# Kernel tuning notes

Hardware: AMD Instinct MI355X
Metric: run time of the kernel (lower is better)

Reference implementation:

```python
import jax, jax.numpy as jnp
import numpy as np

E = 8      # num_expert
D = 1024   # d_model
H = 2048   # expert hidden (htoh4 size)
K = 2      # top_k
N = 2048   # tokens (batch*seq)


def setup_inputs() -> dict:
    key = jax.random.key(0)
    ks = jax.random.split(key, 4)
    sc = lambda k, shape, s: jax.random.normal(k, shape, jnp.float32) * s
    return {
        "inp": jax.random.normal(ks[0], (N, D), jnp.float32),
        "Wg": sc(ks[1], (D, E), D ** -0.5),          # NaiveGate linear
        "bg": jnp.zeros((E,), jnp.float32),
        "W1": sc(ks[2], (E, D, H), D ** -0.5),        # per-expert htoh4
        "b1": jnp.zeros((E, H), jnp.float32),
        "W2": sc(ks[3], (E, H, D), H ** -0.5),        # per-expert h4toh
        "b2": jnp.zeros((E, D), jnp.float32),
    }


def reference(inp, Wg, bg, W1, b1, W2, b2):
    # NaiveGate: linear -> top_k logits -> softmax over the k selected logits
    logits = inp @ Wg + bg                              # [N, E]
    top_val, top_idx = jax.lax.top_k(logits, K)         # [N, K]
    gate_score = jax.nn.softmax(top_val, axis=-1)       # [N, K]

    # Expert grouped compute. Reference computes every expert on every token
    # (exact math, no capacity dropping); combine selects the routed ones.
    h = jax.nn.gelu(jnp.einsum('nd,edh->neh', inp, W1) + b1)   # [N, E, H]
    y = jnp.einsum('neh,ehd->ned', h, W2) + b2                 # [N, E, D]

    # Combine: equivalent to bmm(gate_score[N,1,K], x[N,K,D]) after gather.
    comb = jnp.sum(jax.nn.one_hot(top_idx, E, dtype=inp.dtype)
                   * gate_score[..., None], axis=1)            # [N, E]
    return jnp.einsum('ne,ned->nd', comb, y)                   # [N, D]
```

## Files before the change

kernel.cpp:

```cpp
#include <hip/hip_runtime.h>
#include <math.h>

#define N_TOK 2048
#define DM    1024
#define HD    2048
#define NE    8
#define RMAX  5120
#define TMAX  40

typedef short short8 __attribute__((ext_vector_type(8)));
typedef unsigned short u16x8 __attribute__((ext_vector_type(8)));
typedef float f32x4  __attribute__((ext_vector_type(4)));

__device__ inline unsigned short f2b(float f) {
  unsigned int u = __float_as_uint(f);
  return (unsigned short)((u + 0x7FFFu + ((u >> 16) & 1u)) >> 16);
}
__device__ inline float b2f(unsigned short s) {
  return __uint_as_float(((unsigned int)s) << 16);
}
__device__ inline void gload_lds16(const void* g, void* l) {
  __builtin_amdgcn_global_load_lds(
      (const __attribute__((address_space(1))) unsigned int*)g,
      (__attribute__((address_space(3))) unsigned int*)l, 16, 0, 0);
}

__global__ void gate_kernel(const float* __restrict__ inp,
                            const float* __restrict__ Wg,
                            const float* __restrict__ bg,
                            int* __restrict__ top_idx,
                            float* __restrict__ gate_w) {
  int wave = threadIdx.x >> 6;
  int lane = threadIdx.x & 63;
  int n = blockIdx.x * 4 + wave;
  if (n >= N_TOK) return;
  float acc[NE];
#pragma unroll
  for (int e = 0; e < NE; ++e) acc[e] = 0.f;
  const float4* wg4 = reinterpret_cast<const float4*>(Wg);
#pragma unroll
  for (int i = 0; i < DM / 64; ++i) {
    int d = i * 64 + lane;
    float x = inp[n * DM + d];
    float4 w0 = wg4[d * 2 + 0];
    float4 w1 = wg4[d * 2 + 1];
    acc[0] += x * w0.x; acc[1] += x * w0.y; acc[2] += x * w0.z; acc[3] += x * w0.w;
    acc[4] += x * w1.x; acc[5] += x * w1.y; acc[6] += x * w1.z; acc[7] += x * w1.w;
  }
#pragma unroll
  for (int off = 32; off > 0; off >>= 1) {
#pragma unroll
    for (int e = 0; e < NE; ++e) acc[e] += __shfl_xor(acc[e], off);
  }
  if (lane == 0) {
    float v0 = -1e30f, v1 = -1e30f; int i0 = -1, i1 = -1;
#pragma unroll
    for (int e = 0; e < NE; ++e) {
      float v = acc[e] + bg[e];
      if (v > v0)      { v1 = v0; i1 = i0; v0 = v; i0 = e; }
      else if (v > v1) { v1 = v;  i1 = e; }
    }
    float e1 = expf(v1 - v0);
    float s  = 1.f + e1;
    top_idx[n * 2]     = i0;
    top_idx[n * 2 + 1] = i1;
    gate_w[n * 2]      = 1.f / s;
    gate_w[n * 2 + 1]  = e1 / s;
  }
}

__global__ void group_kernel(const int* __restrict__ top_idx,
                             int* __restrict__ token_of,
                             int* __restrict__ inv_g,
                             int* __restrict__ tile_expert,
                             int* __restrict__ tile_row0,
                             int* __restrict__ n_tiles) {
  __shared__ int s_wtot[4];
  int tid = threadIdx.x, lane = tid & 63, wid = tid >> 6;
  int base = 0, tiles = 0;
  for (int e = 0; e < NE; ++e) {
    int cnt = 0;
    for (int c0 = 0; c0 < N_TOK; c0 += 256) {
      int n = c0 + tid;
      int t0 = top_idx[n * 2], t1 = top_idx[n * 2 + 1];
      bool f = (t0 == e) || (t1 == e);
      int k = (t0 == e) ? 0 : 1;
      unsigned long long m = __ballot(f);
      int lp = __popcll(m & ((1ull << lane) - 1ull));
      if (lane == 0) s_wtot[wid] = __popcll(m);
      __syncthreads();
      int wbase = 0;
      for (int w = 0; w < 4; ++w) if (w < wid) wbase += s_wtot[w];
      if (f) {
        int pos = base + cnt + wbase + lp;
        token_of[pos] = n;
        inv_g[n * 2 + k] = pos;
      }
      cnt += s_wtot[0] + s_wtot[1] + s_wtot[2] + s_wtot[3];
      __syncthreads();
    }
    int padded = (cnt + 127) & ~127;
    for (int i = cnt + tid; i < padded; i += 256) token_of[base + i] = -1;
    if (tid == 0) {
      for (int t = 0; t < padded / 128; ++t) {
        tile_expert[tiles + t] = e;
        tile_row0[tiles + t]   = base + t * 128;
      }
    }
    tiles += padded / 128;
    base  += padded;
    __syncthreads();
  }
  if (tid == 0) n_tiles[0] = tiles;
}

__global__ void xcvt_kernel(const float* __restrict__ inp,
                            unsigned short* __restrict__ Xb) {
  int i = (blockIdx.x * 256 + threadIdx.x) * 8;
  float4 a = *(const float4*)(inp + i);
  float4 b = *(const float4*)(inp + i + 4);
  ushort4 pa, pb;
  pa.x = f2b(a.x); pa.y = f2b(a.y); pa.z = f2b(a.z); pa.w = f2b(a.w);
  pb.x = f2b(b.x); pb.y = f2b(b.y); pb.z = f2b(b.z); pb.w = f2b(b.w);
  *(ushort4*)(Xb + i)     = pa;
  *(ushort4*)(Xb + i + 4) = pb;
}

__global__ __launch_bounds__(256) void wcvt_kernel(
    const float* __restrict__ W1, const float* __restrict__ W2,
    unsigned short* __restrict__ W1C, unsigned short* __restrict__ W2C) {
  int z = blockIdx.z;
  const float* src; unsigned short* dst; int K, N;
  if (z < NE) { src = W1 + (size_t)z * DM * HD; dst = W1C + (size_t)z * DM * HD; K = DM; N = HD; }
  else        { src = W2 + (size_t)(z - NE) * HD * DM; dst = W2C + (size_t)(z - NE) * HD * DM; K = HD; N = DM; }
  int n0 = blockIdx.x * 64, k0 = blockIdx.y * 32;
  if (n0 >= N || k0 >= K) return;
  int t = threadIdx.x;
  int n = t & 63, kg = t >> 6;
  const float* s = src + (size_t)(k0 + kg * 8) * N + n0 + n;
  float v[8];
#pragma unroll
  for (int i = 0; i < 8; ++i) v[i] = s[(size_t)i * N];
  u16x8 o;
#pragma unroll
  for (int i = 0; i < 8; ++i) o[i] = f2b(v[i]);
  *(u16x8*)(dst + ((size_t)(k0 / 8 + kg) * N + n0 + n) * 8) = o;
}

__global__ __launch_bounds__(256) void ffn1_mfma(
    const unsigned short* __restrict__ Xb,
    const unsigned short* __restrict__ W1C,
    const float* __restrict__ b1,
    const unsigned short* __restrict__ zbuf,
    const int* __restrict__ token_of, const int* __restrict__ tile_expert,
    const int* __restrict__ tile_row0, const int* __restrict__ n_tiles,
    unsigned short* __restrict__ Hbuf) {
  if ((int)blockIdx.x >= n_tiles[0]) return;
  int e    = tile_expert[blockIdx.x];
  int row0 = tile_row0[blockIdx.x];
  int h0   = blockIdx.y * 64;
  __shared__ __align__(16) unsigned short Asl[128][32];
  __shared__ __align__(16) unsigned short Bsl[64][32];
  int tid = threadIdx.x, lane = tid & 63;
  int wid = tid >> 6, wr = wid >> 1, wc = wid & 1;
  int l15 = lane & 15, l4 = lane >> 4;
  int sw  = (l15 >> 1) & 3;

  int ar[2], asg[2];
  int tk[2];
#pragma unroll
  for (int q = 0; q < 2; ++q) {
    int idx = tid + q * 256;
    ar[q]  = idx >> 2;
    asg[q] = (idx & 3) ^ ((ar[q] >> 1) & 3);
    tk[q]  = token_of[row0 + ar[q]];
  }
  int bc  = tid >> 2;
  int bsg = (tid & 3) ^ ((bc >> 1) & 3);

  f32x4 acc[4][2] = {};
  const unsigned short* W1e = W1C + (size_t)e * DM * HD;

  for (int kc = 0; kc < DM; kc += 32) {
    __syncthreads();
#pragma unroll
    for (int q = 0; q < 2; ++q) {
      int idx = tid + q * 256;
      const unsigned short* ga = (tk[q] < 0)
          ? zbuf
          : Xb + (size_t)tk[q] * DM + kc + asg[q] * 8;
      gload_lds16(ga, (char*)&Asl[0][0] + (size_t)idx * 16);
    }
    {
      const unsigned short* gb =
          W1e + ((size_t)((kc >> 3) + bsg) * HD + h0 + bc) * 8;
      gload_lds16(gb, (char*)&Bsl[0][0] + (size_t)tid * 16);
    }
    __syncthreads();
    short8 a[4], b[2];
#pragma unroll
    for (int m = 0; m < 4; ++m) {
      int R = wr * 64 + m * 16 + l15;
      a[m] = *(const short8*)((const char*)&Asl[0][0] + R * 64 + ((l4 ^ sw) << 4));
    }
#pragma unroll
    for (int n = 0; n < 2; ++n) {
      int R = wc * 32 + n * 16 + l15;
      b[n] = *(const short8*)((const char*)&Bsl[0][0] + R * 64 + ((l4 ^ sw) << 4));
    }
#pragma unroll
    for (int m = 0; m < 4; ++m)
#pragma unroll
      for (int n = 0; n < 2; ++n)
        acc[m][n] = __builtin_amdgcn_mfma_f32_16x16x32_bf16(a[m], b[n], acc[m][n], 0, 0, 0);
  }

  float bias[2];
#pragma unroll
  for (int n = 0; n < 2; ++n) bias[n] = b1[e * HD + h0 + wc * 32 + n * 16 + l15];
#pragma unroll
  for (int m = 0; m < 4; ++m) {
#pragma unroll
    for (int n = 0; n < 2; ++n) {
      int col = h0 + wc * 32 + n * 16 + l15;
#pragma unroll
      for (int j = 0; j < 4; ++j) {
        int row = row0 + wr * 64 + m * 16 + l4 * 4 + j;
        float x = acc[m][n][j] + bias[n];
        float g = 0.5f * x * (1.f + tanhf(0.7978845608f * (x + 0.044715f * x * x * x)));
        Hbuf[(size_t)row * HD + col] = f2b(g);
      }
    }
  }
}

__global__ __launch_bounds__(256) void ffn2_mfma(
    const unsigned short* __restrict__ Hbuf,
    const unsigned short* __restrict__ W2C,
    const float* __restrict__ b2,
    const int* __restrict__ tile_expert, const int* __restrict__ tile_row0,
    const int* __restrict__ n_tiles,
    unsigned short* __restrict__ Ybuf) {
  if ((int)blockIdx.x >= n_tiles[0]) return;
  int e    = tile_expert[blockIdx.x];
  int row0 = tile_row0[blockIdx.x];
  int d0   = blockIdx.y * 64;
  __shared__ __align__(16) unsigned short Asl[128][32];
  __shared__ __align__(16) unsigned short Bsl[64][32];
  int tid = threadIdx.x, lane = tid & 63;
  int wid = tid >> 6, wr = wid >> 1, wc = wid & 1;
  int l15 = lane & 15, l4 = lane >> 4;
  int sw  = (l15 >> 1) & 3;

  int ar[2], asg[2];
#pragma unroll
  for (int q = 0; q < 2; ++q) {
    int idx = tid + q * 256;
    ar[q]  = idx >> 2;
    asg[q] = (idx & 3) ^ ((ar[q] >> 1) & 3);
  }
  int bc  = tid >> 2;
  int bsg = (tid & 3) ^ ((bc >> 1) & 3);

  f32x4 acc[4][2] = {};
  const unsigned short* W2e = W2C + (size_t)e * DM * HD;

  for (int kc = 0; kc < HD; kc += 32) {
    __syncthreads();
#pragma unroll
    for (int q = 0; q < 2; ++q) {
      int idx = tid + q * 256;
      const unsigned short* ga =
          Hbuf + (size_t)(row0 + ar[q]) * HD + kc + asg[q] * 8;
      gload_lds16(ga, (char*)&Asl[0][0] + (size_t)idx * 16);
    }
    {
      const unsigned short* gb =
          W2e + ((size_t)((kc >> 3) + bsg) * DM + d0 + bc) * 8;
      gload_lds16(gb, (char*)&Bsl[0][0] + (size_t)tid * 16);
    }
    __syncthreads();
    short8 a[4], b[2];
#pragma unroll
    for (int m = 0; m < 4; ++m) {
      int R = wr * 64 + m * 16 + l15;
      a[m] = *(const short8*)((const char*)&Asl[0][0] + R * 64 + ((l4 ^ sw) << 4));
    }
#pragma unroll
    for (int n = 0; n < 2; ++n) {
      int R = wc * 32 + n * 16 + l15;
      b[n] = *(const short8*)((const char*)&Bsl[0][0] + R * 64 + ((l4 ^ sw) << 4));
    }
#pragma unroll
    for (int m = 0; m < 4; ++m)
#pragma unroll
      for (int n = 0; n < 2; ++n)
        acc[m][n] = __builtin_amdgcn_mfma_f32_16x16x32_bf16(a[m], b[n], acc[m][n], 0, 0, 0);
  }

  float bias[2];
#pragma unroll
  for (int n = 0; n < 2; ++n) bias[n] = b2[e * DM + d0 + wc * 32 + n * 16 + l15];
#pragma unroll
  for (int m = 0; m < 4; ++m) {
#pragma unroll
    for (int n = 0; n < 2; ++n) {
      int col = d0 + wc * 32 + n * 16 + l15;
#pragma unroll
      for (int j = 0; j < 4; ++j) {
        int row = row0 + wr * 64 + m * 16 + l4 * 4 + j;
        Ybuf[(size_t)row * DM + col] = f2b(acc[m][n][j] + bias[n]);
      }
    }
  }
}

__global__ void combine_kernel(const unsigned short* __restrict__ Ybuf,
                               const int* __restrict__ inv_g,
                               const float* __restrict__ gate_w,
                               float* __restrict__ out) {
  int n = blockIdx.x;
  int r0 = inv_g[n * 2], r1 = inv_g[n * 2 + 1];
  float g0 = gate_w[n * 2], g1 = gate_w[n * 2 + 1];
  int i = threadIdx.x;
  ushort4 a = *(const ushort4*)(Ybuf + (size_t)r0 * DM + i * 4);
  ushort4 b = *(const ushort4*)(Ybuf + (size_t)r1 * DM + i * 4);
  float4 rv;
  rv.x = g0 * b2f(a.x) + g1 * b2f(b.x);
  rv.y = g0 * b2f(a.y) + g1 * b2f(b.y);
  rv.z = g0 * b2f(a.z) + g1 * b2f(b.z);
  rv.w = g0 * b2f(a.w) + g1 * b2f(b.w);
  *(float4*)(out + (size_t)n * DM + i * 4) = rv;
}

extern "C" void kernel_launch(void* const* d_in, const int* in_sizes, int n_in,
                              void* d_out, int out_size, void* d_ws, size_t ws_size,
                              hipStream_t stream) {
  const float* inp = (const float*)d_in[0];
  const float* Wg  = (const float*)d_in[1];
  const float* bg  = (const float*)d_in[2];
  const float* W1  = (const float*)d_in[3];
  const float* b1  = (const float*)d_in[4];
  const float* W2  = (const float*)d_in[5];
  const float* b2  = (const float*)d_in[6];
  float* out = (float*)d_out;

  char* ws = (char*)d_ws;
  size_t off = 0;
  auto alloc = [&](size_t bytes) {
    size_t o = off;
    off = (off + bytes + 255) & ~(size_t)255;
    return o;
  };
  int*   top_idx     = (int*)  (ws + alloc(N_TOK * 2 * sizeof(int)));
  float* gate_w      = (float*)(ws + alloc(N_TOK * 2 * sizeof(float)));
  int*   token_of    = (int*)  (ws + alloc(RMAX * sizeof(int)));
  int*   inv_g       = (int*)  (ws + alloc(N_TOK * 2 * sizeof(int)));
  int*   tile_expert = (int*)  (ws + alloc(TMAX * sizeof(int)));
  int*   tile_row0   = (int*)  (ws + alloc(TMAX * sizeof(int)));
  int*   n_tiles     = (int*)  (ws + alloc(sizeof(int)));
  unsigned short* zbuf = (unsigned short*)(ws + alloc(256));
  unsigned short* Xb   = (unsigned short*)(ws + alloc((size_t)N_TOK * DM * 2));
  unsigned short* W1C  = (unsigned short*)(ws + alloc((size_t)NE * DM * HD * 2));
  unsigned short* W2C  = (unsigned short*)(ws + alloc((size_t)NE * DM * HD * 2));
  unsigned short* Hbuf = (unsigned short*)(ws + alloc((size_t)RMAX * HD * 2));
  unsigned short* Ybuf = (unsigned short*)(ws + alloc((size_t)RMAX * DM * 2));
  (void)ws_size;

  hipMemsetAsync(zbuf, 0, 256, stream);
  gate_kernel<<<N_TOK / 4, 256, 0, stream>>>(inp, Wg, bg, top_idx, gate_w);
  group_kernel<<<1, 256, 0, stream>>>(top_idx, token_of, inv_g,
                                      tile_expert, tile_row0, n_tiles);
  xcvt_kernel<<<(N_TOK * DM) / (256 * 8), 256, 0, stream>>>(inp, Xb);
  wcvt_kernel<<<dim3(32, 64, 2 * NE), 256, 0, stream>>>(W1, W2, W1C, W2C);
  ffn1_mfma<<<dim3(TMAX, HD / 64), 256, 0, stream>>>(
      Xb, W1C, b1, zbuf, token_of, tile_expert, tile_row0, n_tiles, Hbuf);
  ffn2_mfma<<<dim3(TMAX, DM / 64), 256, 0, stream>>>(
      Hbuf, W2C, b2, tile_expert, tile_row0, n_tiles, Ybuf);
  combine_kernel<<<N_TOK, 256, 0, stream>>>(Ybuf, inv_g, gate_w, out);
}
```

Measured before the change: 165.5 us.

## Fuse gate, input and weight conversion into one prep kernel; widen grouping

Merges the gate, input bf16 conversion and weight conversion kernels into a single launch partitioned by block index. The weight conversion path now reads float4 vectors and writes four packed columns per thread. The grouping kernel uses 1024 threads to cut loop iterations and barriers. This aims to reduce launch overhead and improve memory efficiency of the conversion, at the cost of mixed block types in one grid.

```diff
diff --git a/kernel.cpp b/kernel.cpp
--- a/kernel.cpp
+++ b/kernel.cpp
@@ -8,6 +8,11 @@
 #define RMAX  5120
 #define TMAX  40
 
+#define GATE_BLKS 512
+#define XCVT_BLKS 1024
+#define WCVT_PER  256
+#define PREP_BLKS (GATE_BLKS + XCVT_BLKS + 16 * WCVT_PER)
+
 typedef short short8 __attribute__((ext_vector_type(8)));
 typedef unsigned short u16x8 __attribute__((ext_vector_type(8)));
 typedef float f32x4  __attribute__((ext_vector_type(4)));
@@ -25,62 +30,101 @@
       (__attribute__((address_space(3))) unsigned int*)l, 16, 0, 0);
 }
 
-__global__ void gate_kernel(const float* __restrict__ inp,
-                            const float* __restrict__ Wg,
-                            const float* __restrict__ bg,
-                            int* __restrict__ top_idx,
-                            float* __restrict__ gate_w) {
-  int wave = threadIdx.x >> 6;
-  int lane = threadIdx.x & 63;
-  int n = blockIdx.x * 4 + wave;
-  if (n >= N_TOK) return;
-  float acc[NE];
-#pragma unroll
-  for (int e = 0; e < NE; ++e) acc[e] = 0.f;
-  const float4* wg4 = reinterpret_cast<const float4*>(Wg);
-#pragma unroll
-  for (int i = 0; i < DM / 64; ++i) {
-    int d = i * 64 + lane;
-    float x = inp[n * DM + d];
-    float4 w0 = wg4[d * 2 + 0];
-    float4 w1 = wg4[d * 2 + 1];
-    acc[0] += x * w0.x; acc[1] += x * w0.y; acc[2] += x * w0.z; acc[3] += x * w0.w;
-    acc[4] += x * w1.x; acc[5] += x * w1.y; acc[6] += x * w1.z; acc[7] += x * w1.w;
-  }
-#pragma unroll
-  for (int off = 32; off > 0; off >>= 1) {
-#pragma unroll
-    for (int e = 0; e < NE; ++e) acc[e] += __shfl_xor(acc[e], off);
-  }
-  if (lane == 0) {
-    float v0 = -1e30f, v1 = -1e30f; int i0 = -1, i1 = -1;
-#pragma unroll
-    for (int e = 0; e < NE; ++e) {
-      float v = acc[e] + bg[e];
-      if (v > v0)      { v1 = v0; i1 = i0; v0 = v; i0 = e; }
-      else if (v > v1) { v1 = v;  i1 = e; }
-    }
-    float e1 = expf(v1 - v0);
-    float s  = 1.f + e1;
-    top_idx[n * 2]     = i0;
-    top_idx[n * 2 + 1] = i1;
-    gate_w[n * 2]      = 1.f / s;
-    gate_w[n * 2 + 1]  = e1 / s;
-  }
-}
-
-__global__ void group_kernel(const int* __restrict__ top_idx,
-                             int* __restrict__ token_of,
-                             int* __restrict__ inv_g,
-                             int* __restrict__ tile_expert,
-                             int* __restrict__ tile_row0,
-                             int* __restrict__ n_tiles) {
-  __shared__ int s_wtot[4];
+__global__ __launch_bounds__(256) void prep_kernel(
+    const float* __restrict__ inp, const float* __restrict__ Wg,
+    const float* __restrict__ bg,  const float* __restrict__ W1,
+    const float* __restrict__ W2,
+    int* __restrict__ top_idx, float* __restrict__ gate_w,
+    unsigned short* __restrict__ Xb,
+    unsigned short* __restrict__ W1C, unsigned short* __restrict__ W2C) {
+  int bid = blockIdx.x;
+  if (bid < GATE_BLKS) {
+    int wave = threadIdx.x >> 6;
+    int lane = threadIdx.x & 63;
+    int n = bid * 4 + wave;
+    float acc[NE];
+#pragma unroll
+    for (int e = 0; e < NE; ++e) acc[e] = 0.f;
+    const float4* wg4 = reinterpret_cast<const float4*>(Wg);
+#pragma unroll
+    for (int i = 0; i < DM / 64; ++i) {
+      int d = i * 64 + lane;
+      float x = inp[n * DM + d];
+      float4 w0 = wg4[d * 2 + 0];
+      float4 w1 = wg4[d * 2 + 1];
+      acc[0] += x * w0.x; acc[1] += x * w0.y; acc[2] += x * w0.z; acc[3] += x * w0.w;
+      acc[4] += x * w1.x; acc[5] += x * w1.y; acc[6] += x * w1.z; acc[7] += x * w1.w;
+    }
+#pragma unroll
+    for (int off = 32; off > 0; off >>= 1) {
+#pragma unroll
+      for (int e = 0; e < NE; ++e) acc[e] += __shfl_xor(acc[e], off);
+    }
+    if (lane == 0) {
+      float v0 = -1e30f, v1 = -1e30f; int i0 = -1, i1 = -1;
+#pragma unroll
+      for (int e = 0; e < NE; ++e) {
+        float v = acc[e] + bg[e];
+        if (v > v0)      { v1 = v0; i1 = i0; v0 = v; i0 = e; }
+        else if (v > v1) { v1 = v;  i1 = e; }
+      }
+      float e1 = expf(v1 - v0);
+      float s  = 1.f + e1;
+      top_idx[n * 2]     = i0;
+      top_idx[n * 2 + 1] = i1;
+      gate_w[n * 2]      = 1.f / s;
+      gate_w[n * 2 + 1]  = e1 / s;
+    }
+  } else if (bid < GATE_BLKS + XCVT_BLKS) {
+    int i = ((bid - GATE_BLKS) * 256 + threadIdx.x) * 8;
+    float4 a = *(const float4*)(inp + i);
+    float4 b = *(const float4*)(inp + i + 4);
+    ushort4 pa, pb;
+    pa.x = f2b(a.x); pa.y = f2b(a.y); pa.z = f2b(a.z); pa.w = f2b(a.w);
+    pb.x = f2b(b.x); pb.y = f2b(b.y); pb.z = f2b(b.z); pb.w = f2b(b.w);
+    *(ushort4*)(Xb + i)     = pa;
+    *(ushort4*)(Xb + i + 4) = pb;
+  } else {
+    int wb = bid - (GATE_BLKS + XCVT_BLKS);
+    int z  = wb >> 8;
+    int r  = wb & 255;
+    const float* src; unsigned short* dst; int K, N, gx, gy;
+    if (z < NE) {
+      src = W1 + (size_t)z * DM * HD; dst = W1C + (size_t)z * DM * HD;
+      K = DM; N = HD; gx = r & 7; gy = r >> 3;
+    } else {
+      src = W2 + (size_t)(z - NE) * HD * DM; dst = W2C + (size_t)(z - NE) * HD * DM;
+      K = HD; N = DM; gx = r & 3; gy = r >> 2;
+    }
+    int n0 = gx * 256, k0 = gy * 32;
+    int t  = threadIdx.x;
+    int cg = t & 63, kg = t >> 6;
+    const float* s = src + (size_t)(k0 + kg * 8) * N + n0 + cg * 4;
+    float4 v[8];
+#pragma unroll
+    for (int i = 0; i < 8; ++i) v[i] = *(const float4*)(s + (size_t)i * N);
+#pragma unroll
+    for (int c = 0; c < 4; ++c) {
+      u16x8 o;
+      o[0] = f2b(v[0][c]); o[1] = f2b(v[1][c]); o[2] = f2b(v[2][c]); o[3] = f2b(v[3][c]);
+      o[4] = f2b(v[4][c]); o[5] = f2b(v[5][c]); o[6] = f2b(v[6][c]); o[7] = f2b(v[7][c]);
+      *(u16x8*)(dst + ((size_t)(k0 / 8 + kg) * N + n0 + cg * 4 + c) * 8) = o;
+    }
+  }
+}
+
+__global__ __launch_bounds__(1024) void group_kernel(
+    const int* __restrict__ top_idx,
+    int* __restrict__ token_of, int* __restrict__ inv_g,
+    int* __restrict__ tile_expert, int* __restrict__ tile_row0,
+    int* __restrict__ n_tiles) {
+  __shared__ int s_wtot[16];
   int tid = threadIdx.x, lane = tid & 63, wid = tid >> 6;
   int base = 0, tiles = 0;
   for (int e = 0; e < NE; ++e) {
     int cnt = 0;
-    for (int c0 = 0; c0 < N_TOK; c0 += 256) {
+#pragma unroll
+    for (int c0 = 0; c0 < N_TOK; c0 += 1024) {
       int n = c0 + tid;
       int t0 = top_idx[n * 2], t1 = top_idx[n * 2 + 1];
       bool f = (t0 == e) || (t1 == e);
@@ -89,18 +133,23 @@
       int lp = __popcll(m & ((1ull << lane) - 1ull));
       if (lane == 0) s_wtot[wid] = __popcll(m);
       __syncthreads();
-      int wbase = 0;
-      for (int w = 0; w < 4; ++w) if (w < wid) wbase += s_wtot[w];
+      int wbase = 0, tot = 0;
+#pragma unroll
+      for (int w = 0; w < 16; ++w) {
+        int c = s_wtot[w];
+        if (w < wid) wbase += c;
+        tot += c;
+      }
       if (f) {
         int pos = base + cnt + wbase + lp;
         token_of[pos] = n;
         inv_g[n * 2 + k] = pos;
       }
-      cnt += s_wtot[0] + s_wtot[1] + s_wtot[2] + s_wtot[3];
+      cnt += tot;
       __syncthreads();
     }
     int padded = (cnt + 127) & ~127;
-    for (int i = cnt + tid; i < padded; i += 256) token_of[base + i] = -1;
+    for (int i = cnt + tid; i < padded; i += 1024) token_of[base + i] = -1;
     if (tid == 0) {
       for (int t = 0; t < padded / 128; ++t) {
         tile_expert[tiles + t] = e;
@@ -112,39 +161,6 @@
     __syncthreads();
   }
   if (tid == 0) n_tiles[0] = tiles;
-}
-
-__global__ void xcvt_kernel(const float* __restrict__ inp,
-                            unsigned short* __restrict__ Xb) {
-  int i = (blockIdx.x * 256 + threadIdx.x) * 8;
-  float4 a = *(const float4*)(inp + i);
-  float4 b = *(const float4*)(inp + i + 4);
-  ushort4 pa, pb;
-  pa.x = f2b(a.x); pa.y = f2b(a.y); pa.z = f2b(a.z); pa.w = f2b(a.w);
-  pb.x = f2b(b.x); pb.y = f2b(b.y); pb.z = f2b(b.z); pb.w = f2b(b.w);
-  *(ushort4*)(Xb + i)     = pa;
-  *(ushort4*)(Xb + i + 4) = pb;
-}
-
-__global__ __launch_bounds__(256) void wcvt_kernel(
-    const float* __restrict__ W1, const float* __restrict__ W2,
-    unsigned short* __restrict__ W1C, unsigned short* __restrict__ W2C) {
-  int z = blockIdx.z;
-  const float* src; unsigned short* dst; int K, N;
-  if (z < NE) { src = W1 + (size_t)z * DM * HD; dst = W1C + (size_t)z * DM * HD; K = DM; N = HD; }
-  else        { src = W2 + (size_t)(z - NE) * HD * DM; dst = W2C + (size_t)(z - NE) * HD * DM; K = HD; N = DM; }
-  int n0 = blockIdx.x * 64, k0 = blockIdx.y * 32;
-  if (n0 >= N || k0 >= K) return;
-  int t = threadIdx.x;
-  int n = t & 63, kg = t >> 6;
-  const float* s = src + (size_t)(k0 + kg * 8) * N + n0 + n;
-  float v[8];
-#pragma unroll
-  for (int i = 0; i < 8; ++i) v[i] = s[(size_t)i * N];
-  u16x8 o;
-#pragma unroll
-  for (int i = 0; i < 8; ++i) o[i] = f2b(v[i]);
-  *(u16x8*)(dst + ((size_t)(k0 / 8 + kg) * N + n0 + n) * 8) = o;
 }
 
 __global__ __launch_bounds__(256) void ffn1_mfma(
@@ -368,11 +384,10 @@
   (void)ws_size;
 
   hipMemsetAsync(zbuf, 0, 256, stream);
-  gate_kernel<<<N_TOK / 4, 256, 0, stream>>>(inp, Wg, bg, top_idx, gate_w);
-  group_kernel<<<1, 256, 0, stream>>>(top_idx, token_of, inv_g,
-                                      tile_expert, tile_row0, n_tiles);
-  xcvt_kernel<<<(N_TOK * DM) / (256 * 8), 256, 0, stream>>>(inp, Xb);
-  wcvt_kernel<<<dim3(32, 64, 2 * NE), 256, 0, stream>>>(W1, W2, W1C, W2C);
+  prep_kernel<<<PREP_BLKS, 256, 0, stream>>>(inp, Wg, bg, W1, W2,
+                                             top_idx, gate_w, Xb, W1C, W2C);
+  group_kernel<<<1, 1024, 0, stream>>>(top_idx, token_of, inv_g,
+                                       tile_expert, tile_row0, n_tiles);
   ffn1_mfma<<<dim3(TMAX, HD / 64), 256, 0, stream>>>(
       Xb, W1C, b1, zbuf, token_of, tile_expert, tile_row0, n_tiles, Hbuf);
   ffn2_mfma<<<dim3(TMAX, DM / 64), 256, 0, stream>>>(
```

Result: no change. 166.4 us (+0.6%).
